# Optimization experiments

Hardware: AMD Instinct MI355X
Metric: run time of the kernel (lower is better)

Reference implementation:

```python
import jax, jax.numpy as jnp
import numpy as np

N, E, IN_CH, EDGE_DIM, H, C = 100000, 1600000, 256, 64, 4, 32


def setup_inputs() -> dict:
    key = jax.random.key(0)
    ks = jax.random.split(key, 8)
    x = jax.random.normal(ks[0], (N, IN_CH), dtype=jnp.float32)
    edge_index = jax.random.randint(ks[1], (2, E), 0, N, dtype=jnp.int32)
    edge_attr = jax.random.normal(ks[2], (E, EDGE_DIM), dtype=jnp.float32)
    W = jax.random.normal(ks[3], (IN_CH, H * C), dtype=jnp.float32) * (1.0 / np.sqrt(IN_CH))
    att_src = jax.random.normal(ks[4], (H, C), dtype=jnp.float32) * (1.0 / np.sqrt(C))
    att_dst = jax.random.normal(ks[5], (H, C), dtype=jnp.float32) * (1.0 / np.sqrt(C))
    W_edge = jax.random.normal(ks[6], (EDGE_DIM, H * C), dtype=jnp.float32) * (1.0 / np.sqrt(EDGE_DIM))
    att_edge = jax.random.normal(ks[7], (H, C), dtype=jnp.float32) * (1.0 / np.sqrt(C))
    bias = jnp.zeros((H * C,), dtype=jnp.float32)
    return {"x": x, "edge_index": edge_index, "edge_attr": edge_attr, "W": W,
            "att_src": att_src, "att_dst": att_dst, "W_edge": W_edge,
            "att_edge": att_edge, "bias": bias}


def reference(x, edge_index, edge_attr, W, att_src, att_dst, W_edge, att_edge, bias):
    # PyG GATConv with edge_dim, add_self_loops=True (fill_value='mean'), concat=True, dropout=0
    n = x.shape[0]
    h, c = att_src.shape
    x_proj = (x @ W).reshape(n, h, c)                       # [N,H,C] shared lin for src/dst
    # add self loops; self-loop edge_attr = feature-wise mean of edge_attr
    loop = jnp.arange(n, dtype=edge_index.dtype)
    src = jnp.concatenate([edge_index[0], loop])            # message source j
    dst = jnp.concatenate([edge_index[1], loop])            # aggregation target i
    loop_attr = jnp.broadcast_to(edge_attr.mean(axis=0), (n, edge_attr.shape[1]))
    ea = jnp.concatenate([edge_attr, loop_attr], axis=0)    # [Et,edge_dim]
    e_proj = (ea @ W_edge).reshape(-1, h, c)                # [Et,H,C]
    a_src = jnp.einsum('nhc,hc->nh', x_proj, att_src)       # [N,H]
    a_dst = jnp.einsum('nhc,hc->nh', x_proj, att_dst)
    a_edge = jnp.einsum('ehc,hc->eh', e_proj, att_edge)     # [Et,H]
    alpha = jax.nn.leaky_relu(a_src[src] + a_dst[dst] + a_edge, negative_slope=0.2)
    # scatter-softmax over incoming edges of each target node
    m = jax.ops.segment_max(alpha, dst, num_segments=n)     # [N,H]
    ex = jnp.exp(alpha - m[dst])
    denom = jax.ops.segment_sum(ex, dst, num_segments=n)
    att = ex / jnp.clip(denom, 1e-16)[dst]                  # [Et,H]
    out = jax.ops.segment_sum(att[:, :, None] * x_proj[src], dst, num_segments=n)  # [N,H,C]
    return out.reshape(n, h * c) + bias
```

## Files before the change

### kernel.cpp

```cpp
#include <hip/hip_runtime.h>


__device__ __forceinline__ float4 f4add(float4 a, float4 b) {
    return make_float4(a.x + b.x, a.y + b.y, a.z + b.z, a.w + b.w);
}

__global__ __launch_bounds__(256) void k_edge_vec(const float* __restrict__ W_edge,
                                                  const float* __restrict__ att_edge,
                                                  float* __restrict__ v) {
    int t = threadIdx.x;
    int d = t >> 2, h = t & 3;
    const float* wr = W_edge + d * 128 + h * 32;
    const float* ar = att_edge + h * 32;
    float s = 0.f;
#pragma unroll
    for (int c = 0; c < 32; ++c) s += wr[c] * ar[c];
    v[d * 4 + h] = s;
}

__global__ __launch_bounds__(256) void k_a_edge(const float4* __restrict__ ea4,
                                                const float4* __restrict__ v4,
                                                float4* __restrict__ a_edge4,
                                                float* __restrict__ a_loop_sum,
                                                int E) {
    int tid = threadIdx.x;
    int lane = tid & 63;
    int sub = lane & 15, rq = lane >> 4;
    int wid = blockIdx.x * 4 + (tid >> 6);
    int nw = gridDim.x * 4;
    float4 v0 = v4[sub * 4 + 0], v1 = v4[sub * 4 + 1];
    float4 v2 = v4[sub * 4 + 2], v3 = v4[sub * 4 + 3];
    float4 asum = make_float4(0, 0, 0, 0);
    int nquad = (E + 3) >> 2;
    for (int qd = wid; qd < nquad; qd += nw) {
        int row = qd * 4 + rq;
        float4 p = make_float4(0, 0, 0, 0);
        bool valid = row < E;
        if (valid) {
            float4 ea = ea4[(size_t)row * 16 + sub];
            p.x = ea.x * v0.x + ea.y * v1.x + ea.z * v2.x + ea.w * v3.x;
            p.y = ea.x * v0.y + ea.y * v1.y + ea.z * v2.y + ea.w * v3.y;
            p.z = ea.x * v0.z + ea.y * v1.z + ea.z * v2.z + ea.w * v3.z;
            p.w = ea.x * v0.w + ea.y * v1.w + ea.z * v2.w + ea.w * v3.w;
            asum = f4add(asum, p);
        }
#pragma unroll
        for (int off = 1; off < 16; off <<= 1) {
            p.x += __shfl_xor(p.x, off);
            p.y += __shfl_xor(p.y, off);
            p.z += __shfl_xor(p.z, off);
            p.w += __shfl_xor(p.w, off);
        }
        if (valid && sub == 0) a_edge4[row] = p;
    }
    __shared__ float4 red[256];
    red[tid] = asum;
    __syncthreads();
    for (int s = 128; s > 0; s >>= 1) {
        if (tid < s) red[tid] = f4add(red[tid], red[tid + s]);
        __syncthreads();
    }
    if (tid == 0) {
        atomicAdd(&a_loop_sum[0], red[0].x);
        atomicAdd(&a_loop_sum[1], red[0].y);
        atomicAdd(&a_loop_sum[2], red[0].z);
        atomicAdd(&a_loop_sum[3], red[0].w);
    }
}

__global__ __launch_bounds__(256) void k_gemm(const float* __restrict__ x,
                                              const float* __restrict__ W,
                                              const float* __restrict__ att_src,
                                              const float* __restrict__ att_dst,
                                              float* __restrict__ x_proj,
                                              float* __restrict__ a_src,
                                              float* __restrict__ a_dst,
                                              int N) {
    __shared__ float xs[32 * 64];
    __shared__ float wsh[64 * 128];
    int tid = threadIdx.x;
    int row0 = blockIdx.x * 32;
    int c4 = tid & 31, rt = tid >> 5;
    int col0 = c4 * 4;
    float4 acc[4];
#pragma unroll
    for (int rr = 0; rr < 4; ++rr) acc[rr] = make_float4(0, 0, 0, 0);

    for (int kb = 0; kb < 256; kb += 64) {
#pragma unroll
        for (int i = 0; i < 2; ++i) {
            int fi = tid + i * 256;
            int r = fi >> 4, cc = (fi & 15) * 4;
            int gr = row0 + r;
            if (gr >= N) gr = N - 1;
            float4 xv = *(const float4*)&x[(size_t)gr * 256 + kb + cc];
            *(float4*)&xs[r * 64 + cc] = xv;
        }
#pragma unroll
        for (int i = 0; i < 8; ++i) {
            int fi = tid + i * 256;
            int kr = fi >> 5, cc = (fi & 31) * 4;
            float4 wv = *(const float4*)&W[(size_t)(kb + kr) * 128 + cc];
            *(float4*)&wsh[kr * 128 + cc] = wv;
        }
        __syncthreads();
#pragma unroll
        for (int k4 = 0; k4 < 16; ++k4) {
            float4 xr[4], wv[4];
#pragma unroll
            for (int rr = 0; rr < 4; ++rr)
                xr[rr] = *(const float4*)&xs[(rt * 4 + rr) * 64 + k4 * 4];
#pragma unroll
            for (int ku = 0; ku < 4; ++ku)
                wv[ku] = *(const float4*)&wsh[(k4 * 4 + ku) * 128 + col0];
#pragma unroll
            for (int rr = 0; rr < 4; ++rr) {
                const float xk[4] = {xr[rr].x, xr[rr].y, xr[rr].z, xr[rr].w};
#pragma unroll
                for (int ku = 0; ku < 4; ++ku) {
                    acc[rr].x = fmaf(xk[ku], wv[ku].x, acc[rr].x);
                    acc[rr].y = fmaf(xk[ku], wv[ku].y, acc[rr].y);
                    acc[rr].z = fmaf(xk[ku], wv[ku].z, acc[rr].z);
                    acc[rr].w = fmaf(xk[ku], wv[ku].w, acc[rr].w);
                }
            }
        }
        __syncthreads();
    }
    float4 asw = *(const float4*)&att_src[col0];
    float4 adw = *(const float4*)&att_dst[col0];
    int head = c4 >> 3;
#pragma unroll
    for (int rr = 0; rr < 4; ++rr) {
        int r = row0 + rt * 4 + rr;
        if (r < N) *(float4*)&x_proj[(size_t)r * 128 + col0] = acc[rr];
        float ps = acc[rr].x * asw.x + acc[rr].y * asw.y + acc[rr].z * asw.z + acc[rr].w * asw.w;
        float pd = acc[rr].x * adw.x + acc[rr].y * adw.y + acc[rr].z * adw.z + acc[rr].w * adw.w;
#pragma unroll
        for (int off = 1; off < 8; off <<= 1) {
            ps += __shfl_xor(ps, off);
            pd += __shfl_xor(pd, off);
        }
        if ((c4 & 7) == 0 && r < N) {
            a_src[r * 4 + head] = ps;
            a_dst[r * 4 + head] = pd;
        }
    }
}

__global__ __launch_bounds__(256) void k_hist(const int* __restrict__ dst,
                                              int* __restrict__ counts, int E) {
    int i = blockIdx.x * blockDim.x + threadIdx.x;
    int stride = gridDim.x * blockDim.x;
    for (; i < E; i += stride) atomicAdd(&counts[dst[i]], 1);
}

__global__ __launch_bounds__(256) void k_scanA(const int* __restrict__ counts,
                                               int* __restrict__ bsum, int N) {
    int b = blockIdx.x, t = threadIdx.x;
    int i0 = b * 1024 + t * 4;
    int s = 0;
    if (i0 + 3 < N) {
        int4 c = *(const int4*)&counts[i0];
        s = c.x + c.y + c.z + c.w;
    } else {
        for (int j = 0; j < 4; ++j)
            if (i0 + j < N) s += counts[i0 + j];
    }
#pragma unroll
    for (int off = 32; off > 0; off >>= 1) s += __shfl_down(s, off);
    __shared__ int wsum[4];
    if ((t & 63) == 0) wsum[t >> 6] = s;
    __syncthreads();
    if (t == 0) bsum[b] = wsum[0] + wsum[1] + wsum[2] + wsum[3];
}

__global__ __launch_bounds__(128) void k_scanB(const int* __restrict__ bsum,
                                               int* __restrict__ boff,
                                               int* __restrict__ row_ptr,
                                               int NB, int N) {
    __shared__ int sh[128];
    int t = threadIdx.x;
    int v = (t < NB) ? bsum[t] : 0;
    sh[t] = v;
    __syncthreads();
    for (int off = 1; off < 128; off <<= 1) {
        int val = sh[t];
        int add = (t >= off) ? sh[t - off] : 0;
        __syncthreads();
        sh[t] = val + add;
        __syncthreads();
    }
    int incl = sh[t];
    if (t < NB) boff[t] = incl - v;
    if (t == NB - 1) row_ptr[N] = incl;
}

__global__ __launch_bounds__(256) void k_scanC(const int* __restrict__ counts,
                                               const int* __restrict__ boff,
                                               int* __restrict__ row_ptr, int N) {
    __shared__ int sh[256];
    int b = blockIdx.x, t = threadIdx.x;
    int i0 = b * 1024 + t * 4;
    int c[4];
    int ts = 0;
#pragma unroll
    for (int j = 0; j < 4; ++j) {
        c[j] = (i0 + j < N) ? counts[i0 + j] : 0;
        ts += c[j];
    }
    sh[t] = ts;
    __syncthreads();
    for (int off = 1; off < 256; off <<= 1) {
        int val = sh[t];
        int add = (t >= off) ? sh[t - off] : 0;
        __syncthreads();
        sh[t] = val + add;
        __syncthreads();
    }
    int run = sh[t] - ts + boff[b];
#pragma unroll
    for (int j = 0; j < 4; ++j) {
        if (i0 + j < N) row_ptr[i0 + j] = run;
        run += c[j];
    }
}

__global__ __launch_bounds__(256) void k_fill(const int* __restrict__ src,
                                              const int* __restrict__ dst,
                                              const float4* __restrict__ a_src4,
                                              const float4* __restrict__ a_dst4,
                                              const float4* __restrict__ a_edge4,
                                              const int* __restrict__ row_ptr,
                                              int* __restrict__ cursor,
                                              int* __restrict__ csr_src,
                                              float4* __restrict__ exp_csr, int E) {
    int i = blockIdx.x * blockDim.x + threadIdx.x;
    int stride = gridDim.x * blockDim.x;
    for (; i < E; i += stride) {
        int d = dst[i], s = src[i];
        int pos = row_ptr[d] + atomicAdd(&cursor[d], 1);
        csr_src[pos] = s;
        float4 a = a_src4[s], b = a_dst4[d], e = a_edge4[i];
        float4 r;
        float t;
        t = a.x + b.x + e.x; t = t > 0.f ? t : 0.2f * t; r.x = __expf(t);
        t = a.y + b.y + e.y; t = t > 0.f ? t : 0.2f * t; r.y = __expf(t);
        t = a.z + b.z + e.z; t = t > 0.f ? t : 0.2f * t; r.z = __expf(t);
        t = a.w + b.w + e.w; t = t > 0.f ? t : 0.2f * t; r.w = __expf(t);
        exp_csr[pos] = r;
    }
}

__global__ __launch_bounds__(256) void k_aggr(const float2* __restrict__ xp2,
                                              const int* __restrict__ row_ptr,
                                              const int* __restrict__ csr_src,
                                              const float* __restrict__ exp_csr,
                                              const float* __restrict__ a_src,
                                              const float* __restrict__ a_dst,
                                              const float* __restrict__ a_loop_sum,
                                              const float* __restrict__ bias,
                                              float* __restrict__ out,
                                              int N, float invE) {
    int lane = threadIdx.x & 63;
    int node = blockIdx.x * 4 + (threadIdx.x >> 6);
    if (node >= N) return;
    int head = lane >> 4;
    int st = row_ptr[node], en = row_ptr[node + 1];
    float aself = a_src[node * 4 + head] + a_dst[node * 4 + head] + a_loop_sum[head] * invE;
    aself = aself > 0.f ? aself : 0.2f * aself;
    float es = __expf(aself);
    float den = es;
    for (int p = st; p < en; ++p) den += exp_csr[(size_t)p * 4 + head];
    float inv = 1.f / den;
    float2 xv = xp2[(size_t)node * 64 + lane];
    float w0 = es * inv;
    float2 acc = make_float2(w0 * xv.x, w0 * xv.y);
    for (int p = st; p < en; ++p) {
        float w = exp_csr[(size_t)p * 4 + head] * inv;
        int s = csr_src[p];
        float2 q = xp2[(size_t)s * 64 + lane];
        acc.x = fmaf(w, q.x, acc.x);
        acc.y = fmaf(w, q.y, acc.y);
    }
    float2 bv = ((const float2*)bias)[lane];
    ((float2*)out)[(size_t)node * 64 + lane] = make_float2(acc.x + bv.x, acc.y + bv.y);
}

extern "C" void kernel_launch(void* const* d_in, const int* in_sizes, int n_in,
                              void* d_out, int out_size, void* d_ws, size_t ws_size,
                              hipStream_t stream) {
    const float* x = (const float*)d_in[0];
    const int* ei = (const int*)d_in[1];
    const float* ea = (const float*)d_in[2];
    const float* W = (const float*)d_in[3];
    const float* att_src = (const float*)d_in[4];
    const float* att_dst = (const float*)d_in[5];
    const float* W_edge = (const float*)d_in[6];
    const float* att_edge = (const float*)d_in[7];
    const float* bias = (const float*)d_in[8];
    float* out = (float*)d_out;

    const int N = in_sizes[0] / 256;
    const int E = in_sizes[1] / 2;
    const int* src = ei;
    const int* dst = ei + E;

    char* base = (char*)d_ws;
    size_t off = 0;
    auto carve = [&](size_t bytes) -> void* {
        off = (off + 15) & ~(size_t)15;
        void* p = base + off;
        off += bytes;
        return p;
    };
    float* a_loop_sum = (float*)carve(16);
    int* counts = (int*)carve((size_t)N * 4);
    int* cursor = (int*)carve((size_t)N * 4);
    size_t zero_bytes = off;
    float* v = (float*)carve(256 * 4);
    int* row_ptr = (int*)carve((size_t)(N + 1) * 4);
    int* bsum = (int*)carve(512);
    int* boff = (int*)carve(512);
    float* a_edge = (float*)carve((size_t)E * 16);
    float* x_proj = (float*)carve((size_t)N * 128 * 4);
    float* a_src = (float*)carve((size_t)N * 16);
    float* a_dst = (float*)carve((size_t)N * 16);
    int* csr_src = (int*)carve((size_t)E * 4);
    float* exp_csr = (float*)carve((size_t)E * 16);
    (void)ws_size;

    hipMemsetAsync(d_ws, 0, zero_bytes, stream);

    k_edge_vec<<<1, 256, 0, stream>>>(W_edge, att_edge, v);
    k_a_edge<<<1024, 256, 0, stream>>>((const float4*)ea, (const float4*)v,
                                       (float4*)a_edge, a_loop_sum, E);
    k_gemm<<<(N + 31) / 32, 256, 0, stream>>>(x, W, att_src, att_dst,
                                              x_proj, a_src, a_dst, N);
    k_hist<<<(E + 255) / 256, 256, 0, stream>>>(dst, counts, E);
    int NB = (N + 1023) / 1024;
    k_scanA<<<NB, 256, 0, stream>>>(counts, bsum, N);
    k_scanB<<<1, 128, 0, stream>>>(bsum, boff, row_ptr, NB, N);
    k_scanC<<<NB, 256, 0, stream>>>(counts, boff, row_ptr, N);
    k_fill<<<(E + 255) / 256, 256, 0, stream>>>(src, dst, (const float4*)a_src,
                                                (const float4*)a_dst, (const float4*)a_edge,
                                                row_ptr, cursor, csr_src,
                                                (float4*)exp_csr, E);
    k_aggr<<<(N + 3) / 4, 256, 0, stream>>>((const float2*)x_proj, row_ptr, csr_src,
                                            exp_csr, a_src, a_dst, a_loop_sum, bias,
                                            out, N, 1.0f / (float)E);
}
```

Measured before the change: 1.170 ms.

## Pack CSR weights and sources into records; fuse softmax denominator into single aggregation pass

Interleaves the per-edge exp weights and source index into one 32-byte record, so the aggregation reads one structure per edge instead of two separate arrays. The denominator and weighted sum are now computed in a single pass, with normalization applied once at the end, which removes the second traversal of the edge list. The inner loop is unrolled by four to keep more gathers of projected features in flight. In exchange the record carries 12 bytes of padding, which raises the size of the CSR buffer and the bytes written by the fill kernel.

Result: faster. 1.055 ms (-9.9%).

```diff
diff --git a/kernel.cpp b/kernel.cpp
--- a/kernel.cpp
+++ b/kernel.cpp
@@ -1,5 +1,7 @@
 #include <hip/hip_runtime.h>
 
+
+struct __align__(16) Rec { float4 w; int4 meta; };
 
 __device__ __forceinline__ float4 f4add(float4 a, float4 b) {
     return make_float4(a.x + b.x, a.y + b.y, a.z + b.z, a.w + b.w);
@@ -233,14 +235,12 @@
                                               const float4* __restrict__ a_edge4,
                                               const int* __restrict__ row_ptr,
                                               int* __restrict__ cursor,
-                                              int* __restrict__ csr_src,
-                                              float4* __restrict__ exp_csr, int E) {
+                                              Rec* __restrict__ recs, int E) {
     int i = blockIdx.x * blockDim.x + threadIdx.x;
     int stride = gridDim.x * blockDim.x;
     for (; i < E; i += stride) {
         int d = dst[i], s = src[i];
         int pos = row_ptr[d] + atomicAdd(&cursor[d], 1);
-        csr_src[pos] = s;
         float4 a = a_src4[s], b = a_dst4[d], e = a_edge4[i];
         float4 r;
         float t;
@@ -248,14 +248,14 @@
         t = a.y + b.y + e.y; t = t > 0.f ? t : 0.2f * t; r.y = __expf(t);
         t = a.z + b.z + e.z; t = t > 0.f ? t : 0.2f * t; r.z = __expf(t);
         t = a.w + b.w + e.w; t = t > 0.f ? t : 0.2f * t; r.w = __expf(t);
-        exp_csr[pos] = r;
+        recs[pos].w = r;
+        recs[pos].meta = make_int4(s, 0, 0, 0);
     }
 }
 
 __global__ __launch_bounds__(256) void k_aggr(const float2* __restrict__ xp2,
                                               const int* __restrict__ row_ptr,
-                                              const int* __restrict__ csr_src,
-                                              const float* __restrict__ exp_csr,
+                                              const Rec* __restrict__ recs,
                                               const float* __restrict__ a_src,
                                               const float* __restrict__ a_dst,
                                               const float* __restrict__ a_loop_sum,
@@ -267,24 +267,48 @@
     if (node >= N) return;
     int head = lane >> 4;
     int st = row_ptr[node], en = row_ptr[node + 1];
+    float den = 0.f;
+    float2 acc = make_float2(0.f, 0.f);
+    int p = st;
+    for (; p + 4 <= en; p += 4) {
+        const float* r0 = (const float*)&recs[p];
+        const float* r1 = (const float*)&recs[p + 1];
+        const float* r2 = (const float*)&recs[p + 2];
+        const float* r3 = (const float*)&recs[p + 3];
+        float w0 = r0[head], w1 = r1[head], w2 = r2[head], w3 = r3[head];
+        int s0 = ((const int*)r0)[4];
+        int s1 = ((const int*)r1)[4];
+        int s2 = ((const int*)r2)[4];
+        int s3 = ((const int*)r3)[4];
+        float2 q0 = xp2[(size_t)s0 * 64 + lane];
+        float2 q1 = xp2[(size_t)s1 * 64 + lane];
+        float2 q2 = xp2[(size_t)s2 * 64 + lane];
+        float2 q3 = xp2[(size_t)s3 * 64 + lane];
+        acc.x = fmaf(w0, q0.x, acc.x); acc.y = fmaf(w0, q0.y, acc.y);
+        acc.x = fmaf(w1, q1.x, acc.x); acc.y = fmaf(w1, q1.y, acc.y);
+        acc.x = fmaf(w2, q2.x, acc.x); acc.y = fmaf(w2, q2.y, acc.y);
+        acc.x = fmaf(w3, q3.x, acc.x); acc.y = fmaf(w3, q3.y, acc.y);
+        den += (w0 + w1) + (w2 + w3);
+    }
+    for (; p < en; ++p) {
+        const float* r0 = (const float*)&recs[p];
+        float w = r0[head];
+        int s = ((const int*)r0)[4];
+        float2 q = xp2[(size_t)s * 64 + lane];
+        acc.x = fmaf(w, q.x, acc.x); acc.y = fmaf(w, q.y, acc.y);
+        den += w;
+    }
     float aself = a_src[node * 4 + head] + a_dst[node * 4 + head] + a_loop_sum[head] * invE;
     aself = aself > 0.f ? aself : 0.2f * aself;
     float es = __expf(aself);
-    float den = es;
-    for (int p = st; p < en; ++p) den += exp_csr[(size_t)p * 4 + head];
+    den += es;
+    float2 xv = xp2[(size_t)node * 64 + lane];
+    acc.x = fmaf(es, xv.x, acc.x);
+    acc.y = fmaf(es, xv.y, acc.y);
     float inv = 1.f / den;
-    float2 xv = xp2[(size_t)node * 64 + lane];
-    float w0 = es * inv;
-    float2 acc = make_float2(w0 * xv.x, w0 * xv.y);
-    for (int p = st; p < en; ++p) {
-        float w = exp_csr[(size_t)p * 4 + head] * inv;
-        int s = csr_src[p];
-        float2 q = xp2[(size_t)s * 64 + lane];
-        acc.x = fmaf(w, q.x, acc.x);
-        acc.y = fmaf(w, q.y, acc.y);
-    }
     float2 bv = ((const float2*)bias)[lane];
-    ((float2*)out)[(size_t)node * 64 + lane] = make_float2(acc.x + bv.x, acc.y + bv.y);
+    ((float2*)out)[(size_t)node * 64 + lane] =
+        make_float2(fmaf(acc.x, inv, bv.x), fmaf(acc.y, inv, bv.y));
 }
 
 extern "C" void kernel_launch(void* const* d_in, const int* in_sizes, int n_in,
@@ -326,8 +350,7 @@
     float* x_proj = (float*)carve((size_t)N * 128 * 4);
     float* a_src = (float*)carve((size_t)N * 16);
     float* a_dst = (float*)carve((size_t)N * 16);
-    int* csr_src = (int*)carve((size_t)E * 4);
-    float* exp_csr = (float*)carve((size_t)E * 16);
+    Rec* recs = (Rec*)carve((size_t)E * sizeof(Rec));
     (void)ws_size;
 
     hipMemsetAsync(d_ws, 0, zero_bytes, stream);
@@ -344,9 +367,8 @@
     k_scanC<<<NB, 256, 0, stream>>>(counts, boff, row_ptr, N);
     k_fill<<<(E + 255) / 256, 256, 0, stream>>>(src, dst, (const float4*)a_src,
                                                 (const float4*)a_dst, (const float4*)a_edge,
-                                                row_ptr, cursor, csr_src,
-                                                (float4*)exp_csr, E);
-    k_aggr<<<(N + 3) / 4, 256, 0, stream>>>((const float2*)x_proj, row_ptr, csr_src,
-                                            exp_csr, a_src, a_dst, a_loop_sum, bias,
+                                                row_ptr, cursor, recs, E);
+    k_aggr<<<(N + 3) / 4, 256, 0, stream>>>((const float2*)x_proj, row_ptr, recs,
+                                            a_src, a_dst, a_loop_sum, bias,
                                             out, N, 1.0f / (float)E);
 }
```
